# Kernel optimization log

Measured on AMD Instinct MI355X. Metric: run time of the kernel, lower is better.

## Reference

```python
import jax, jax.numpy as jnp
import numpy as np

B, NGT, NC, A = 16, 32, 80, 3
STRIDES = (8, 16, 32)
IMG = 640
FEATS = tuple(IMG // s for s in STRIDES)
ANCHOR_SIZES = (((12.0, 16.0), (19.0, 36.0), (40.0, 28.0)),
                ((36.0, 75.0), (76.0, 55.0), (72.0, 146.0)),
                ((142.0, 110.0), (192.0, 243.0), (459.0, 401.0)))
BOX_W, OBJ_W, CLS_W = 0.05, 1.0, 0.5


def _make_anchors(stride, hw, sizes):
    # [A, H, W, 4] in (cx, cy, w, h), centers at cell centers in pixels
    ys = (jnp.arange(hw, dtype=jnp.float32) + 0.5) * stride
    xs = (jnp.arange(hw, dtype=jnp.float32) + 0.5) * stride
    cy, cx = jnp.meshgrid(ys, xs, indexing="ij")
    per = [jnp.stack([cx, cy, jnp.full_like(cx, aw), jnp.full_like(cx, ah)], -1)
           for (aw, ah) in sizes]
    return jnp.stack(per, 0)


def setup_inputs():
    key = jax.random.key(0)
    ks = jax.random.split(key, 8)
    inp = {}
    for i, hw in enumerate(FEATS):
        inp[f"p{i}"] = jax.random.normal(ks[i], (B, A, hw, hw, 5 + NC), dtype=jnp.float32)
        inp[f"a{i}"] = _make_anchors(float(STRIDES[i]), hw, ANCHOR_SIZES[i])
    c = jax.random.uniform(ks[3], (B, NGT, 2), minval=0.0, maxval=float(IMG))
    wh = jax.random.uniform(ks[4], (B, NGT, 2), minval=10.0, maxval=150.0)
    x1y1 = jnp.clip(c - wh / 2, 0.0, IMG - 2.0)
    x2y2 = jnp.clip(c + wh / 2, x1y1 + 1.0, float(IMG))
    inp["gt_boxes"] = jnp.concatenate([x1y1, x2y2], axis=-1)  # [B, NGT, 4] xyxy pixels
    inp["gt_labels"] = jax.random.randint(ks[5], (B, NGT), 0, NC).astype(jnp.int32)
    return inp


def _bce_logits(x, t):
    # BCEWithLogits, elementwise: softplus(x) - x*t
    return jax.nn.softplus(x) - x * t


def _assign_image(gt_b, gt_l, anchors, stride):
    # gt_b: [N,4] xyxy, gt_l: [N], anchors: [A,H,W,4] cxcywh
    Aa, H, W, _ = anchors.shape
    N = gt_b.shape[0]
    cx = (gt_b[:, 0] + gt_b[:, 2]) * 0.5
    cy = (gt_b[:, 1] + gt_b[:, 3]) * 0.5
    gx = jnp.clip((cx / stride).astype(jnp.int32), 0, W - 1)
    gy = jnp.clip((cy / stride).astype(jnp.int32), 0, H - 1)
    cell = jnp.transpose(anchors[:, gy, gx, :], (1, 0, 2))  # [N, A, 4] cxcywh
    c1 = cell[..., :2] - cell[..., 2:] * 0.5
    c2 = cell[..., :2] + cell[..., 2:] * 0.5
    lt = jnp.maximum(gt_b[:, None, :2], c1)
    rb = jnp.minimum(gt_b[:, None, 2:], c2)
    whi = jnp.maximum(rb - lt, 0.0)
    inter = whi[..., 0] * whi[..., 1]
    area1 = (gt_b[:, 2] - gt_b[:, 0]) * (gt_b[:, 3] - gt_b[:, 1])
    area2 = cell[..., 2] * cell[..., 3]
    iou = inter / (area1[:, None] + area2 - inter + 1e-16)  # [N, A]
    best_a = jnp.argmax(iou, axis=1).astype(jnp.int32)
    best_iou = jnp.take_along_axis(iou, best_a[:, None], axis=1)[:, 0]
    K = Aa * H * W
    keyidx = best_a * (H * W) + gy * W + gx  # [N], flat (anchor, gy, gx) key
    best_per_key = jnp.zeros((K,), iou.dtype).at[keyidx].max(best_iou)
    is_winner = best_iou >= best_per_key[keyidx]
    cand = jnp.where(is_winner, jnp.arange(N, dtype=jnp.int32), N)
    chosen = jnp.full((K,), N, dtype=jnp.int32).at[keyidx].min(cand)
    mask = chosen < N
    cg = jnp.clip(chosen, 0, N - 1)
    gb = gt_b[cg]                      # [K, 4]
    anc = anchors.reshape(K, 4)        # flat order matches key = a*H*W + gy*W + gx
    gcx = (gb[:, 0] + gb[:, 2]) * 0.5
    gcy = (gb[:, 1] + gb[:, 3]) * 0.5
    gw = gb[:, 2] - gb[:, 0]
    gh = gb[:, 3] - gb[:, 1]
    s0 = float(STRIDES[0])  # NOTE: original uses strides[0] for ALL scales (faithful)
    tx = (gcx - anc[:, 0]) / s0
    ty = (gcy - anc[:, 1]) / s0
    tw = jnp.log(gw / anc[:, 2] + 1e-16)
    th = jnp.log(gh / anc[:, 3] + 1e-16)
    box_t = jnp.where(mask[:, None], jnp.stack([tx, ty, tw, th], axis=-1), 0.0)
    obj_t = mask.astype(jnp.float32)
    cls_t = jax.nn.one_hot(gt_l[cg], NC, dtype=jnp.float32) * mask[:, None]
    return box_t, obj_t, cls_t


def _forward(preds, ancs, gt_boxes, gt_labels):
    tb = jnp.float32(0.0)
    to = jnp.float32(0.0)
    tc = jnp.float32(0.0)
    tot_pos = jnp.float32(0.0)
    for pred, anchors, stride in zip(preds, ancs, STRIDES):
        b, a, h, w, _ = pred.shape
        flat = pred.reshape(b, a * h * w, 5 + NC)
        box_p, obj_p, cls_p = flat[..., :4], flat[..., 4], flat[..., 5:]
        box_t, obj_t, cls_t = jax.vmap(
            lambda gb, gl: _assign_image(gb, gl, anchors, float(stride))
        )(gt_boxes, gt_labels)
        pos = obj_t > 0
        npos = pos.sum().astype(jnp.float32)
        denom = jnp.maximum(npos, 1.0)
        box_l = jnp.sum(((box_p - box_t) ** 2).sum(-1) * pos) / denom
        obj_l = jnp.mean(_bce_logits(obj_p, obj_t))
        cls_l = jnp.sum(_bce_logits(cls_p, cls_t) * pos[..., None]) / (denom * NC)
        tb = tb + jnp.where(npos > 0, box_l, 0.0)
        tc = tc + jnp.where(npos > 0, cls_l, 0.0)
        to = to + obj_l
        tot_pos = tot_pos + npos
    ns = float(len(STRIDES))
    tb = jnp.where(tot_pos > 0, tb / ns, 0.0)
    tc = jnp.where(tot_pos > 0, tc / ns, 0.0)
    to = to / ns
    return BOX_W * tb + OBJ_W * to + CLS_W * tc


def reference(p0, p1, p2, a0, a1, a2, gt_boxes, gt_labels):
    return _forward((p0, p1, p2), (a0, a1, a2), gt_boxes, gt_labels)
```

## Files before the change

kernel.cpp:

```cpp
#include <hip/hip_runtime.h>
#include <math.h>

#define NLEV 3
#define BATCH 16
#define NGT 32
#define NCLS 80
#define NA 3

#define P0 307200
#define P1 76800
#define P2 19200

#define OBJ_NB0 300
#define OBJ_NB1 75
#define OBJ_NB2 19
#define OBJ_NB  (OBJ_NB0 + OBJ_NB1 + OBJ_NB2)
#define OBJ_B0  OBJ_NB0
#define OBJ_B01 (OBJ_NB0 + OBJ_NB1)

#define NASSIGN (BATCH * NLEV)
#define NB (NASSIGN + OBJ_NB)

#define ASSIGN_OFF 4096

__device__ __forceinline__ float softplusf(float x) {
    return fmaxf(x, 0.0f) + log1pf(expf(-fabsf(x)));
}

__global__ void fused_kernel(const float* __restrict__ p0, const float* __restrict__ p1,
                             const float* __restrict__ p2,
                             const float* __restrict__ gtb, const int* __restrict__ gtl,
                             float* __restrict__ ws) {
    const int blk = blockIdx.x;
    const int tid = threadIdx.x;
    const int wid = tid >> 6, lane = tid & 63;

    __shared__ float wsum[4];
    __shared__ int      s_key[NGT];
    __shared__ float    s_iou[NGT];
    __shared__ unsigned s_off[NGT];
    __shared__ float    s_t[NGT][4];
    __shared__ int      s_lab[NGT];
    __shared__ float    s_np;
    __shared__ float    s_red[4][3];

    if (blk >= NASSIGN) {
        const int ob = blk - NASSIGN;
        const float* p;
        int base, plim;
        if (ob < OBJ_NB0)      { p = p0; base = ob * 1024;               plim = P0; }
        else if (ob < OBJ_B01) { p = p1; base = (ob - OBJ_NB0) * 1024;   plim = P1; }
        else                   { p = p2; base = (ob - OBJ_B01) * 1024;   plim = P2; }

        float x[4];
        #pragma unroll
        for (int k = 0; k < 4; ++k) {
            int pos = base + k * 256 + tid;
            pos = (pos < plim) ? pos : (plim - 1);
            x[k] = __builtin_nontemporal_load(&p[(size_t)pos * (5 + NCLS) + 4]);
        }
        float v = 0.0f;
        #pragma unroll
        for (int k = 0; k < 4; ++k) {
            const int pos = base + k * 256 + tid;
            v += (pos < plim) ? softplusf(x[k]) : 0.0f;
        }
        for (int off = 32; off > 0; off >>= 1) v += __shfl_down(v, off);
        if (lane == 0) wsum[wid] = v;
        __syncthreads();
        if (tid == 0) ws[ob] = wsum[0] + wsum[1] + wsum[2] + wsum[3];
        return;
    }

    const int aid = blk;
    const int lev = aid % NLEV;
    const int b   = aid / NLEV;

    const float* pred = (lev == 0) ? p0 : ((lev == 1) ? p1 : p2);
    const int   W      = (lev == 0) ? 80 : ((lev == 1) ? 40 : 20);
    const float stride = (lev == 0) ? 8.0f : ((lev == 1) ? 16.0f : 32.0f);
    const int H = W;
    const int HW = H * W;
    const float aw0 = (lev == 0) ? 12.f  : ((lev == 1) ? 36.f : 142.f);
    const float ah0 = (lev == 0) ? 16.f  : ((lev == 1) ? 75.f : 110.f);
    const float aw1 = (lev == 0) ? 19.f  : ((lev == 1) ? 76.f : 192.f);
    const float ah1 = (lev == 0) ? 36.f  : ((lev == 1) ? 55.f : 243.f);
    const float aw2 = (lev == 0) ? 40.f  : ((lev == 1) ? 72.f : 459.f);
    const float ah2 = (lev == 0) ? 28.f  : ((lev == 1) ? 146.f : 401.f);

    float x1 = 0.f, y1 = 0.f, x2 = 0.f, y2 = 0.f, cx = 0.f, cy = 0.f;
    float acx = 0.f, acy = 0.f;
    float biou = -1.0f;
    int ba = 0, gx = 0, gy = 0, key = -1, lab = 0;

    if (tid < NGT) {
        const float4 g = ((const float4*)gtb)[b * NGT + tid];
        lab = gtl[b * NGT + tid];
        x1 = g.x; y1 = g.y; x2 = g.z; y2 = g.w;
        cx = (x1 + x2) * 0.5f;
        cy = (y1 + y2) * 0.5f;
        gx = (int)(cx / stride); gx = gx < 0 ? 0 : (gx > W - 1 ? W - 1 : gx);
        gy = (int)(cy / stride); gy = gy < 0 ? 0 : (gy > H - 1 ? H - 1 : gy);
        acx = ((float)gx + 0.5f) * stride;
        acy = ((float)gy + 0.5f) * stride;
        const float area1 = (x2 - x1) * (y2 - y1);
        #pragma unroll
        for (int aa = 0; aa < NA; ++aa) {
            const float aw = (aa == 0) ? aw0 : ((aa == 1) ? aw1 : aw2);
            const float ah = (aa == 0) ? ah0 : ((aa == 1) ? ah1 : ah2);
            const float c1x = acx - aw * 0.5f, c1y = acy - ah * 0.5f;
            const float c2x = acx + aw * 0.5f, c2y = acy + ah * 0.5f;
            const float ltx = fmaxf(x1, c1x), lty = fmaxf(y1, c1y);
            const float rbx = fminf(x2, c2x), rby = fminf(y2, c2y);
            const float wx = fmaxf(rbx - ltx, 0.0f), wy = fmaxf(rby - lty, 0.0f);
            const float inter = wx * wy;
            const float iou = inter / (area1 + aw * ah - inter + 1e-16f);
            if (iou > biou) { biou = iou; ba = aa; }
        }
        key = ba * HW + gy * W + gx;
        s_key[tid] = key;
        s_iou[tid] = biou;
    }
    __syncthreads();

    if (tid < NGT) {
        bool chosen = true;
        for (int m = 0; m < NGT; ++m) {
            if (m == tid) continue;
            if (s_key[m] == key) {
                const float im = s_iou[m];
                if (im > biou || (im == biou && m < tid)) chosen = false;
            }
        }
        if (chosen) {
            const float aw = (ba == 0) ? aw0 : ((ba == 1) ? aw1 : aw2);
            const float ah = (ba == 0) ? ah0 : ((ba == 1) ? ah1 : ah2);
            s_t[tid][0] = (cx - acx) * 0.125f;
            s_t[tid][1] = (cy - acy) * 0.125f;
            s_t[tid][2] = logf((x2 - x1) / aw + 1e-16f);
            s_t[tid][3] = logf((y2 - y1) / ah + 1e-16f);
            s_lab[tid]  = lab;
            s_off[tid]  = (unsigned)(((b * NA + ba) * HW + gy * W + gx) * (5 + NCLS));
        } else {
            s_t[tid][0] = 0.f; s_t[tid][1] = 0.f; s_t[tid][2] = 0.f; s_t[tid][3] = 0.f;
            s_lab[tid] = -1;
            s_off[tid] = 0xFFFFFFFFu;
        }
        const unsigned long long mm = __ballot(chosen);
        if (tid == 0) s_np = (float)__popcll(mm);
    }
    __syncthreads();

    unsigned offs[8];
    int      labs[8];
    #pragma unroll
    for (int k = 0; k < 8; ++k) {
        offs[k] = s_off[wid * 8 + k];
        labs[k] = s_lab[wid * 8 + k];
    }

    float accO = 0.f, accB = 0.f, accC = 0.f;
    #pragma unroll
    for (int k = 0; k < 8; ++k) {
        const int g = wid * 8 + k;
        const bool ok = (offs[k] != 0xFFFFFFFFu);
        const float* f = pred + (ok ? offs[k] : 0u);
        const int idx1 = (lane < 21) ? (lane + 64) : 0;
        const float v0 = f[lane];
        const float v1 = f[idx1];
        const float tv = s_t[g][lane & 3];
        const int glab = labs[k];

        const float d = v0 - tv;
        accB += (ok && lane < 4)  ? d * d : 0.0f;
        accO += (ok && lane == 4) ? v0    : 0.0f;
        const float c0 = softplusf(v0) - ((lane - 5 == glab) ? v0 : 0.0f);
        accC += (ok && lane >= 5) ? c0 : 0.0f;
        const float c1 = softplusf(v1) - ((lane + 59 == glab) ? v1 : 0.0f);
        accC += (ok && lane < 21) ? c1 : 0.0f;
    }

    for (int off = 32; off > 0; off >>= 1) {
        accO += __shfl_down(accO, off);
        accB += __shfl_down(accB, off);
        accC += __shfl_down(accC, off);
    }
    if (lane == 0) { s_red[wid][0] = accO; s_red[wid][1] = accB; s_red[wid][2] = accC; }
    __syncthreads();
    if (tid == 0) {
        float* dst = ws + ASSIGN_OFF + (size_t)aid * 4;
        dst[0] = s_red[0][0] + s_red[1][0] + s_red[2][0] + s_red[3][0];
        dst[1] = s_red[0][1] + s_red[1][1] + s_red[2][1] + s_red[3][1];
        dst[2] = s_red[0][2] + s_red[1][2] + s_red[2][2] + s_red[3][2];
        dst[3] = s_np;
    }
}

__global__ void finalize_kernel(const float* __restrict__ ws, float* __restrict__ out) {
    const int tid = threadIdx.x;
    const int lane = tid & 63, wid = tid >> 6;

    float a0 = 0.f, a1 = 0.f, a2 = 0.f;
    for (int i = tid; i < OBJ_NB; i += 256) {
        const float v = ws[i];
        if (i < OBJ_B0)       a0 += v;
        else if (i < OBJ_B01) a1 += v;
        else                  a2 += v;
    }
    for (int off = 32; off > 0; off >>= 1) {
        a0 += __shfl_down(a0, off);
        a1 += __shfl_down(a1, off);
        a2 += __shfl_down(a2, off);
    }
    __shared__ float red[4][3];
    if (lane == 0) { red[wid][0] = a0; red[wid][1] = a1; red[wid][2] = a2; }

    __shared__ float ared[4][NLEV];
    if (wid == 1) {
        float po = 0.f, bx = 0.f, cl = 0.f, np = 0.f;
        int l = 0;
        if (lane < NASSIGN) {
            const float* src = ws + ASSIGN_OFF + (size_t)lane * 4;
            po = src[0]; bx = src[1]; cl = src[2]; np = src[3];
            l = lane % NLEV;
        }
        for (int lv = 0; lv < NLEV; ++lv) {
            float vpo = (l == lv && lane < NASSIGN) ? po : 0.f;
            float vbx = (l == lv && lane < NASSIGN) ? bx : 0.f;
            float vcl = (l == lv && lane < NASSIGN) ? cl : 0.f;
            float vnp = (l == lv && lane < NASSIGN) ? np : 0.f;
            for (int off = 32; off > 0; off >>= 1) {
                vpo += __shfl_down(vpo, off);
                vbx += __shfl_down(vbx, off);
                vcl += __shfl_down(vcl, off);
                vnp += __shfl_down(vnp, off);
            }
            if (lane == 0) { ared[0][lv] = vpo; ared[1][lv] = vbx; ared[2][lv] = vcl; ared[3][lv] = vnp; }
        }
    }
    __syncthreads();

    if (tid == 0) {
        const float BK0 = (float)P0, BK1 = (float)P1, BK2 = (float)P2;
        float tb = 0.f, to = 0.f, tc = 0.f, tot = 0.f;
        for (int l = 0; l < NLEV; ++l) {
            const float BKl = (l == 0) ? BK0 : ((l == 1) ? BK1 : BK2);
            const float sp = red[0][l] + red[1][l] + red[2][l] + red[3][l];
            const float po = ared[0][l], bx = ared[1][l], cl = ared[2][l], np = ared[3][l];
            const float denom = fmaxf(np, 1.0f);
            const float obj_l = (sp - po) / BKl;
            const float box_l = bx / denom;
            const float cls_l = cl / (denom * (float)NCLS);
            if (np > 0.f) { tb += box_l; tc += cls_l; }
            to += obj_l;
            tot += np;
        }
        if (tot > 0.f) { tb /= 3.0f; tc /= 3.0f; } else { tb = 0.f; tc = 0.f; }
        to /= 3.0f;
        out[0] = 0.05f * tb + 1.0f * to + 0.5f * tc;
    }
}

extern "C" void kernel_launch(void* const* d_in, const int* in_sizes, int n_in,
                              void* d_out, int out_size, void* d_ws, size_t ws_size,
                              hipStream_t stream) {
    const float* p[3] = {nullptr, nullptr, nullptr};
    const float* gtb = nullptr;
    const int*   gtl = nullptr;
    for (int i = 0; i < n_in; ++i) {
        switch (in_sizes[i]) {
            case 26112000: p[0] = (const float*)d_in[i]; break;
            case 6528000:  p[1] = (const float*)d_in[i]; break;
            case 1632000:  p[2] = (const float*)d_in[i]; break;
            case 2048:     gtb  = (const float*)d_in[i]; break;
            case 512:      gtl  = (const int*)d_in[i];   break;
            default: break;
        }
    }
    if (!p[0]) p[0] = (const float*)d_in[0];
    if (!p[1]) p[1] = (const float*)d_in[2];
    if (!p[2]) p[2] = (const float*)d_in[4];
    if (!gtb)  gtb  = (const float*)d_in[6];
    if (!gtl)  gtl  = (const int*)d_in[7];

    float* ws = (float*)d_ws;

    fused_kernel<<<NB, 256, 0, stream>>>(p[0], p[1], p[2], gtb, gtl, ws);
    finalize_kernel<<<1, 256, 0, stream>>>(ws, (float*)d_out);
}
```

Before: 18.98 us.

## Fold finalize reduction into main kernel with a last-block atomic counter

Removes the separate finalize kernel launch. Each block bumps a global counter after publishing its partial sum, and the last block to arrive reads all partials with agent-scope atomic loads and writes the final loss. The counter is reset each call with a hipMemsetAsync, which adds its own small stream operation and relies on correct fence ordering. It also replaces the nontemporal objectness loads with plain loads and drops the barrier between the IoU-key write and the duplicate-resolution read, since all 32 GT threads sit in one wavefront.

Measured after the change: 32.67 us. 1.72x slower.

```diff
diff --git a/kernel.cpp b/kernel.cpp
--- a/kernel.cpp
+++ b/kernel.cpp
@@ -22,15 +22,20 @@
 #define NB (NASSIGN + OBJ_NB)
 
 #define ASSIGN_OFF 4096
+#define CNT_BYTE_OFF 32768
 
 __device__ __forceinline__ float softplusf(float x) {
     return fmaxf(x, 0.0f) + log1pf(expf(-fabsf(x)));
+}
+
+__device__ __forceinline__ float coh_load(const float* p) {
+    return __hip_atomic_load(p, __ATOMIC_RELAXED, __HIP_MEMORY_SCOPE_AGENT);
 }
 
 __global__ void fused_kernel(const float* __restrict__ p0, const float* __restrict__ p1,
                              const float* __restrict__ p2,
                              const float* __restrict__ gtb, const int* __restrict__ gtl,
-                             float* __restrict__ ws) {
+                             float* __restrict__ ws, float* __restrict__ out) {
     const int blk = blockIdx.x;
     const int tid = threadIdx.x;
     const int wid = tid >> 6, lane = tid & 63;
@@ -43,6 +48,11 @@
     __shared__ int      s_lab[NGT];
     __shared__ float    s_np;
     __shared__ float    s_red[4][3];
+    __shared__ unsigned s_lastf;
+    __shared__ float    f_red[4][3];
+    __shared__ float    f_ared[4][NLEV];
+
+    unsigned* cnt = (unsigned*)((char*)ws + CNT_BYTE_OFF);
 
     if (blk >= NASSIGN) {
         const int ob = blk - NASSIGN;
@@ -57,7 +67,7 @@
         for (int k = 0; k < 4; ++k) {
             int pos = base + k * 256 + tid;
             pos = (pos < plim) ? pos : (plim - 1);
-            x[k] = __builtin_nontemporal_load(&p[(size_t)pos * (5 + NCLS) + 4]);
+            x[k] = p[(size_t)pos * (5 + NCLS) + 4];
         }
         float v = 0.0f;
         #pragma unroll
@@ -69,195 +79,191 @@
         if (lane == 0) wsum[wid] = v;
         __syncthreads();
         if (tid == 0) ws[ob] = wsum[0] + wsum[1] + wsum[2] + wsum[3];
-        return;
-    }
-
-    const int aid = blk;
-    const int lev = aid % NLEV;
-    const int b   = aid / NLEV;
-
-    const float* pred = (lev == 0) ? p0 : ((lev == 1) ? p1 : p2);
-    const int   W      = (lev == 0) ? 80 : ((lev == 1) ? 40 : 20);
-    const float stride = (lev == 0) ? 8.0f : ((lev == 1) ? 16.0f : 32.0f);
-    const int H = W;
-    const int HW = H * W;
-    const float aw0 = (lev == 0) ? 12.f  : ((lev == 1) ? 36.f : 142.f);
-    const float ah0 = (lev == 0) ? 16.f  : ((lev == 1) ? 75.f : 110.f);
-    const float aw1 = (lev == 0) ? 19.f  : ((lev == 1) ? 76.f : 192.f);
-    const float ah1 = (lev == 0) ? 36.f  : ((lev == 1) ? 55.f : 243.f);
-    const float aw2 = (lev == 0) ? 40.f  : ((lev == 1) ? 72.f : 459.f);
-    const float ah2 = (lev == 0) ? 28.f  : ((lev == 1) ? 146.f : 401.f);
-
-    float x1 = 0.f, y1 = 0.f, x2 = 0.f, y2 = 0.f, cx = 0.f, cy = 0.f;
-    float acx = 0.f, acy = 0.f;
-    float biou = -1.0f;
-    int ba = 0, gx = 0, gy = 0, key = -1, lab = 0;
-
-    if (tid < NGT) {
-        const float4 g = ((const float4*)gtb)[b * NGT + tid];
-        lab = gtl[b * NGT + tid];
-        x1 = g.x; y1 = g.y; x2 = g.z; y2 = g.w;
-        cx = (x1 + x2) * 0.5f;
-        cy = (y1 + y2) * 0.5f;
-        gx = (int)(cx / stride); gx = gx < 0 ? 0 : (gx > W - 1 ? W - 1 : gx);
-        gy = (int)(cy / stride); gy = gy < 0 ? 0 : (gy > H - 1 ? H - 1 : gy);
-        acx = ((float)gx + 0.5f) * stride;
-        acy = ((float)gy + 0.5f) * stride;
-        const float area1 = (x2 - x1) * (y2 - y1);
-        #pragma unroll
-        for (int aa = 0; aa < NA; ++aa) {
-            const float aw = (aa == 0) ? aw0 : ((aa == 1) ? aw1 : aw2);
-            const float ah = (aa == 0) ? ah0 : ((aa == 1) ? ah1 : ah2);
-            const float c1x = acx - aw * 0.5f, c1y = acy - ah * 0.5f;
-            const float c2x = acx + aw * 0.5f, c2y = acy + ah * 0.5f;
-            const float ltx = fmaxf(x1, c1x), lty = fmaxf(y1, c1y);
-            const float rbx = fminf(x2, c2x), rby = fminf(y2, c2y);
-            const float wx = fmaxf(rbx - ltx, 0.0f), wy = fmaxf(rby - lty, 0.0f);
-            const float inter = wx * wy;
-            const float iou = inter / (area1 + aw * ah - inter + 1e-16f);
-            if (iou > biou) { biou = iou; ba = aa; }
-        }
-        key = ba * HW + gy * W + gx;
-        s_key[tid] = key;
-        s_iou[tid] = biou;
+    } else {
+        const int aid = blk;
+        const int lev = aid % NLEV;
+        const int b   = aid / NLEV;
+
+        const float* pred = (lev == 0) ? p0 : ((lev == 1) ? p1 : p2);
+        const int   W      = (lev == 0) ? 80 : ((lev == 1) ? 40 : 20);
+        const float stride = (lev == 0) ? 8.0f : ((lev == 1) ? 16.0f : 32.0f);
+        const int H = W;
+        const int HW = H * W;
+        const float aw0 = (lev == 0) ? 12.f  : ((lev == 1) ? 36.f : 142.f);
+        const float ah0 = (lev == 0) ? 16.f  : ((lev == 1) ? 75.f : 110.f);
+        const float aw1 = (lev == 0) ? 19.f  : ((lev == 1) ? 76.f : 192.f);
+        const float ah1 = (lev == 0) ? 36.f  : ((lev == 1) ? 55.f : 243.f);
+        const float aw2 = (lev == 0) ? 40.f  : ((lev == 1) ? 72.f : 459.f);
+        const float ah2 = (lev == 0) ? 28.f  : ((lev == 1) ? 146.f : 401.f);
+
+        if (tid < NGT) {
+            const float4 g = ((const float4*)gtb)[b * NGT + tid];
+            const int lab = gtl[b * NGT + tid];
+            const float x1 = g.x, y1 = g.y, x2 = g.z, y2 = g.w;
+            const float cx = (x1 + x2) * 0.5f;
+            const float cy = (y1 + y2) * 0.5f;
+            int gx = (int)(cx / stride); gx = gx < 0 ? 0 : (gx > W - 1 ? W - 1 : gx);
+            int gy = (int)(cy / stride); gy = gy < 0 ? 0 : (gy > H - 1 ? H - 1 : gy);
+            const float acx = ((float)gx + 0.5f) * stride;
+            const float acy = ((float)gy + 0.5f) * stride;
+            const float area1 = (x2 - x1) * (y2 - y1);
+            float biou = -1.0f;
+            int ba = 0;
+            #pragma unroll
+            for (int aa = 0; aa < NA; ++aa) {
+                const float aw = (aa == 0) ? aw0 : ((aa == 1) ? aw1 : aw2);
+                const float ah = (aa == 0) ? ah0 : ((aa == 1) ? ah1 : ah2);
+                const float c1x = acx - aw * 0.5f, c1y = acy - ah * 0.5f;
+                const float c2x = acx + aw * 0.5f, c2y = acy + ah * 0.5f;
+                const float ltx = fmaxf(x1, c1x), lty = fmaxf(y1, c1y);
+                const float rbx = fminf(x2, c2x), rby = fminf(y2, c2y);
+                const float wx = fmaxf(rbx - ltx, 0.0f), wy = fmaxf(rby - lty, 0.0f);
+                const float inter = wx * wy;
+                const float iou = inter / (area1 + aw * ah - inter + 1e-16f);
+                if (iou > biou) { biou = iou; ba = aa; }
+            }
+            const int key = ba * HW + gy * W + gx;
+            s_key[tid] = key;
+            s_iou[tid] = biou;
+
+            bool chosen = true;
+            for (int m = 0; m < NGT; ++m) {
+                if (m == tid) continue;
+                if (s_key[m] == key) {
+                    const float im = s_iou[m];
+                    if (im > biou || (im == biou && m < tid)) chosen = false;
+                }
+            }
+            if (chosen) {
+                const float aw = (ba == 0) ? aw0 : ((ba == 1) ? aw1 : aw2);
+                const float ah = (ba == 0) ? ah0 : ((ba == 1) ? ah1 : ah2);
+                s_t[tid][0] = (cx - acx) * 0.125f;
+                s_t[tid][1] = (cy - acy) * 0.125f;
+                s_t[tid][2] = logf((x2 - x1) / aw + 1e-16f);
+                s_t[tid][3] = logf((y2 - y1) / ah + 1e-16f);
+                s_lab[tid]  = lab;
+                s_off[tid]  = (unsigned)(((b * NA + ba) * HW + gy * W + gx) * (5 + NCLS));
+            } else {
+                s_t[tid][0] = 0.f; s_t[tid][1] = 0.f; s_t[tid][2] = 0.f; s_t[tid][3] = 0.f;
+                s_lab[tid] = -1;
+                s_off[tid] = 0xFFFFFFFFu;
+            }
+            const unsigned long long mm = __ballot(chosen);
+            if (tid == 0) s_np = (float)__popcll(mm);
+        }
+        __syncthreads();
+
+        unsigned offs[8];
+        int      labs[8];
+        #pragma unroll
+        for (int k = 0; k < 8; ++k) {
+            offs[k] = s_off[wid * 8 + k];
+            labs[k] = s_lab[wid * 8 + k];
+        }
+
+        float accO = 0.f, accB = 0.f, accC = 0.f;
+        #pragma unroll
+        for (int k = 0; k < 8; ++k) {
+            const int g = wid * 8 + k;
+            const bool ok = (offs[k] != 0xFFFFFFFFu);
+            const float* f = pred + (ok ? offs[k] : 0u);
+            const int idx1 = (lane < 21) ? (lane + 64) : 0;
+            const float v0 = f[lane];
+            const float v1 = f[idx1];
+            const float tv = s_t[g][lane & 3];
+            const int glab = labs[k];
+
+            const float d = v0 - tv;
+            accB += (ok && lane < 4)  ? d * d : 0.0f;
+            accO += (ok && lane == 4) ? v0    : 0.0f;
+            const float c0 = softplusf(v0) - ((lane - 5 == glab) ? v0 : 0.0f);
+            accC += (ok && lane >= 5) ? c0 : 0.0f;
+            const float c1 = softplusf(v1) - ((lane + 59 == glab) ? v1 : 0.0f);
+            accC += (ok && lane < 21) ? c1 : 0.0f;
+        }
+
+        for (int off = 32; off > 0; off >>= 1) {
+            accO += __shfl_down(accO, off);
+            accB += __shfl_down(accB, off);
+            accC += __shfl_down(accC, off);
+        }
+        if (lane == 0) { s_red[wid][0] = accO; s_red[wid][1] = accB; s_red[wid][2] = accC; }
+        __syncthreads();
+        if (tid == 0) {
+            float* dst = ws + ASSIGN_OFF + (size_t)aid * 4;
+            dst[0] = s_red[0][0] + s_red[1][0] + s_red[2][0] + s_red[3][0];
+            dst[1] = s_red[0][1] + s_red[1][1] + s_red[2][1] + s_red[3][1];
+            dst[2] = s_red[0][2] + s_red[1][2] + s_red[2][2] + s_red[3][2];
+            dst[3] = s_np;
+        }
+    }
+
+    if (tid == 0) {
+        __threadfence();
+        const unsigned done = atomicAdd(cnt, 1u);
+        s_lastf = (done == NB - 1) ? 1u : 0u;
     }
     __syncthreads();
-
-    if (tid < NGT) {
-        bool chosen = true;
-        for (int m = 0; m < NGT; ++m) {
-            if (m == tid) continue;
-            if (s_key[m] == key) {
-                const float im = s_iou[m];
-                if (im > biou || (im == biou && m < tid)) chosen = false;
-            }
-        }
-        if (chosen) {
-            const float aw = (ba == 0) ? aw0 : ((ba == 1) ? aw1 : aw2);
-            const float ah = (ba == 0) ? ah0 : ((ba == 1) ? ah1 : ah2);
-            s_t[tid][0] = (cx - acx) * 0.125f;
-            s_t[tid][1] = (cy - acy) * 0.125f;
-            s_t[tid][2] = logf((x2 - x1) / aw + 1e-16f);
-            s_t[tid][3] = logf((y2 - y1) / ah + 1e-16f);
-            s_lab[tid]  = lab;
-            s_off[tid]  = (unsigned)(((b * NA + ba) * HW + gy * W + gx) * (5 + NCLS));
-        } else {
-            s_t[tid][0] = 0.f; s_t[tid][1] = 0.f; s_t[tid][2] = 0.f; s_t[tid][3] = 0.f;
-            s_lab[tid] = -1;
-            s_off[tid] = 0xFFFFFFFFu;
-        }
-        const unsigned long long mm = __ballot(chosen);
-        if (tid == 0) s_np = (float)__popcll(mm);
-    }
-    __syncthreads();
-
-    unsigned offs[8];
-    int      labs[8];
-    #pragma unroll
-    for (int k = 0; k < 8; ++k) {
-        offs[k] = s_off[wid * 8 + k];
-        labs[k] = s_lab[wid * 8 + k];
-    }
-
-    float accO = 0.f, accB = 0.f, accC = 0.f;
-    #pragma unroll
-    for (int k = 0; k < 8; ++k) {
-        const int g = wid * 8 + k;
-        const bool ok = (offs[k] != 0xFFFFFFFFu);
-        const float* f = pred + (ok ? offs[k] : 0u);
-        const int idx1 = (lane < 21) ? (lane + 64) : 0;
-        const float v0 = f[lane];
-        const float v1 = f[idx1];
-        const float tv = s_t[g][lane & 3];
-        const int glab = labs[k];
-
-        const float d = v0 - tv;
-        accB += (ok && lane < 4)  ? d * d : 0.0f;
-        accO += (ok && lane == 4) ? v0    : 0.0f;
-        const float c0 = softplusf(v0) - ((lane - 5 == glab) ? v0 : 0.0f);
-        accC += (ok && lane >= 5) ? c0 : 0.0f;
-        const float c1 = softplusf(v1) - ((lane + 59 == glab) ? v1 : 0.0f);
-        accC += (ok && lane < 21) ? c1 : 0.0f;
-    }
-
-    for (int off = 32; off > 0; off >>= 1) {
-        accO += __shfl_down(accO, off);
-        accB += __shfl_down(accB, off);
-        accC += __shfl_down(accC, off);
-    }
-    if (lane == 0) { s_red[wid][0] = accO; s_red[wid][1] = accB; s_red[wid][2] = accC; }
-    __syncthreads();
-    if (tid == 0) {
-        float* dst = ws + ASSIGN_OFF + (size_t)aid * 4;
-        dst[0] = s_red[0][0] + s_red[1][0] + s_red[2][0] + s_red[3][0];
-        dst[1] = s_red[0][1] + s_red[1][1] + s_red[2][1] + s_red[3][1];
-        dst[2] = s_red[0][2] + s_red[1][2] + s_red[2][2] + s_red[3][2];
-        dst[3] = s_np;
-    }
-}
-
-__global__ void finalize_kernel(const float* __restrict__ ws, float* __restrict__ out) {
-    const int tid = threadIdx.x;
-    const int lane = tid & 63, wid = tid >> 6;
-
-    float a0 = 0.f, a1 = 0.f, a2 = 0.f;
-    for (int i = tid; i < OBJ_NB; i += 256) {
-        const float v = ws[i];
-        if (i < OBJ_B0)       a0 += v;
-        else if (i < OBJ_B01) a1 += v;
-        else                  a2 += v;
-    }
-    for (int off = 32; off > 0; off >>= 1) {
-        a0 += __shfl_down(a0, off);
-        a1 += __shfl_down(a1, off);
-        a2 += __shfl_down(a2, off);
-    }
-    __shared__ float red[4][3];
-    if (lane == 0) { red[wid][0] = a0; red[wid][1] = a1; red[wid][2] = a2; }
-
-    __shared__ float ared[4][NLEV];
-    if (wid == 1) {
-        float po = 0.f, bx = 0.f, cl = 0.f, np = 0.f;
-        int l = 0;
-        if (lane < NASSIGN) {
-            const float* src = ws + ASSIGN_OFF + (size_t)lane * 4;
-            po = src[0]; bx = src[1]; cl = src[2]; np = src[3];
-            l = lane % NLEV;
-        }
-        for (int lv = 0; lv < NLEV; ++lv) {
-            float vpo = (l == lv && lane < NASSIGN) ? po : 0.f;
-            float vbx = (l == lv && lane < NASSIGN) ? bx : 0.f;
-            float vcl = (l == lv && lane < NASSIGN) ? cl : 0.f;
-            float vnp = (l == lv && lane < NASSIGN) ? np : 0.f;
-            for (int off = 32; off > 0; off >>= 1) {
-                vpo += __shfl_down(vpo, off);
-                vbx += __shfl_down(vbx, off);
-                vcl += __shfl_down(vcl, off);
-                vnp += __shfl_down(vnp, off);
-            }
-            if (lane == 0) { ared[0][lv] = vpo; ared[1][lv] = vbx; ared[2][lv] = vcl; ared[3][lv] = vnp; }
-        }
-    }
-    __syncthreads();
-
-    if (tid == 0) {
-        const float BK0 = (float)P0, BK1 = (float)P1, BK2 = (float)P2;
-        float tb = 0.f, to = 0.f, tc = 0.f, tot = 0.f;
-        for (int l = 0; l < NLEV; ++l) {
-            const float BKl = (l == 0) ? BK0 : ((l == 1) ? BK1 : BK2);
-            const float sp = red[0][l] + red[1][l] + red[2][l] + red[3][l];
-            const float po = ared[0][l], bx = ared[1][l], cl = ared[2][l], np = ared[3][l];
-            const float denom = fmaxf(np, 1.0f);
-            const float obj_l = (sp - po) / BKl;
-            const float box_l = bx / denom;
-            const float cls_l = cl / (denom * (float)NCLS);
-            if (np > 0.f) { tb += box_l; tc += cls_l; }
-            to += obj_l;
-            tot += np;
-        }
-        if (tot > 0.f) { tb /= 3.0f; tc /= 3.0f; } else { tb = 0.f; tc = 0.f; }
-        to /= 3.0f;
-        out[0] = 0.05f * tb + 1.0f * to + 0.5f * tc;
+    if (s_lastf) {
+        __threadfence();
+
+        float a0 = 0.f, a1 = 0.f, a2 = 0.f;
+        for (int i = tid; i < OBJ_NB; i += 256) {
+            const float v = coh_load(&ws[i]);
+            if (i < OBJ_B0)       a0 += v;
+            else if (i < OBJ_B01) a1 += v;
+            else                  a2 += v;
+        }
+        for (int off = 32; off > 0; off >>= 1) {
+            a0 += __shfl_down(a0, off);
+            a1 += __shfl_down(a1, off);
+            a2 += __shfl_down(a2, off);
+        }
+        if (lane == 0) { f_red[wid][0] = a0; f_red[wid][1] = a1; f_red[wid][2] = a2; }
+
+        if (wid == 1) {
+            float po = 0.f, bx = 0.f, cl = 0.f, np = 0.f;
+            int l = 0;
+            if (lane < NASSIGN) {
+                const float* src = ws + ASSIGN_OFF + (size_t)lane * 4;
+                po = coh_load(&src[0]); bx = coh_load(&src[1]);
+                cl = coh_load(&src[2]); np = coh_load(&src[3]);
+                l = lane % NLEV;
+            }
+            for (int lv = 0; lv < NLEV; ++lv) {
+                float vpo = (l == lv && lane < NASSIGN) ? po : 0.f;
+                float vbx = (l == lv && lane < NASSIGN) ? bx : 0.f;
+                float vcl = (l == lv && lane < NASSIGN) ? cl : 0.f;
+                float vnp = (l == lv && lane < NASSIGN) ? np : 0.f;
+                for (int off = 32; off > 0; off >>= 1) {
+                    vpo += __shfl_down(vpo, off);
+                    vbx += __shfl_down(vbx, off);
+                    vcl += __shfl_down(vcl, off);
+                    vnp += __shfl_down(vnp, off);
+                }
+                if (lane == 0) { f_ared[0][lv] = vpo; f_ared[1][lv] = vbx; f_ared[2][lv] = vcl; f_ared[3][lv] = vnp; }
+            }
+        }
+        __syncthreads();
+
+        if (tid == 0) {
+            float tb = 0.f, to = 0.f, tc = 0.f, tot = 0.f;
+            for (int l = 0; l < NLEV; ++l) {
+                const float BKl = (l == 0) ? (float)P0 : ((l == 1) ? (float)P1 : (float)P2);
+                const float sp = f_red[0][l] + f_red[1][l] + f_red[2][l] + f_red[3][l];
+                const float po = f_ared[0][l], bx = f_ared[1][l], cl = f_ared[2][l], np = f_ared[3][l];
+                const float denom = fmaxf(np, 1.0f);
+                const float obj_l = (sp - po) / BKl;
+                const float box_l = bx / denom;
+                const float cls_l = cl / (denom * (float)NCLS);
+                if (np > 0.f) { tb += box_l; tc += cls_l; }
+                to += obj_l;
+                tot += np;
+            }
+            if (tot > 0.f) { tb /= 3.0f; tc /= 3.0f; } else { tb = 0.f; tc = 0.f; }
+            to /= 3.0f;
+            out[0] = 0.05f * tb + 1.0f * to + 0.5f * tc;
+        }
     }
 }
 
@@ -285,6 +291,6 @@
 
     float* ws = (float*)d_ws;
 
-    fused_kernel<<<NB, 256, 0, stream>>>(p[0], p[1], p[2], gtb, gtl, ws);
-    finalize_kernel<<<1, 256, 0, stream>>>(ws, (float*)d_out);
-}
+    hipMemsetAsync((char*)d_ws + CNT_BYTE_OFF, 0, 4, stream);
+    fused_kernel<<<NB, 256, 0, stream>>>(p[0], p[1], p[2], gtb, gtl, ws, (float*)d_out);
+}
```
